# Kernel optimization log

Measured on AMD Instinct MI355X. Metric: run time of the kernel, lower is better.

Reference implementation:

```python
import jax, jax.numpy as jnp
import numpy as np

EPS = 1e-12  # matches torch.nn.functional.normalize eps


def setup_inputs() -> dict:
    key = jax.random.key(0)
    inputs = jax.random.normal(key, (128, 64, 64, 32), dtype=jnp.float32)
    return {"inputs": inputs}


def reference(inputs) -> jnp.ndarray:
    B, N = inputs.shape[0], inputs.shape[1]
    x = inputs.reshape(B, N, -1)                       # (B, N, D)
    norm = jnp.linalg.norm(x, axis=2, keepdims=True)   # (B, N, 1)
    att = x / jnp.maximum(norm, EPS)                   # L2-normalized rows
    # full N x N self-similarity per batch element
    sim = jnp.einsum('bnd,bmd->bnm', att, att)         # (B, N, N)
    diag_mean = (att * att).sum(axis=2).sum(axis=1).mean()
    loss = sim.sum(axis=(1, 2)).mean() - diag_mean
    return loss
```

## Files before the change

### kernel.cpp

```cpp
#include <hip/hip_runtime.h>
#include <math.h>

#define BB 128
#define NN 64
#define DD 2048
#define NBLK1 512
#define SEG 4

typedef float f4 __attribute__((ext_vector_type(4)));

__device__ __forceinline__ float wave_reduce_sum_down(float v) {
    #pragma unroll
    for (int off = 32; off > 0; off >>= 1)
        v += __shfl_down(v, off, 64);
    return v;
}

__global__ __launch_bounds__(256) void stream_kernel(
        const float* __restrict__ x,
        float* __restrict__ vseg,
        float* __restrict__ diag_seg,
        unsigned* __restrict__ counter) {
    const int u = blockIdx.x;
    const int b = u >> 2, s = u & 3;
    const int t = threadIdx.x;
    const int lane = t & 63, w = t >> 6;

    if (u == 0 && t == 0) *counter = 0;

    const float* xw = x + ((size_t)b * NN + s * 16 + w * 4) * DD;

    f4 a[4][8];
    #pragma unroll
    for (int r = 0; r < 4; ++r) {
        const f4* p = reinterpret_cast<const f4*>(xw + (size_t)r * DD);
        #pragma unroll
        for (int j = 0; j < 8; ++j)
            a[r][j] = __builtin_nontemporal_load(&p[lane + 64 * j]);
    }

    float ss[4];
    #pragma unroll
    for (int r = 0; r < 4; ++r) {
        float s4 = 0.f;
        #pragma unroll
        for (int j = 0; j < 8; ++j)
            s4 += a[r][j].x * a[r][j].x + a[r][j].y * a[r][j].y
                + a[r][j].z * a[r][j].z + a[r][j].w * a[r][j].w;
        ss[r] = s4;
    }

    #pragma unroll
    for (int off = 1; off < 64; off <<= 1) {
        float s0 = __shfl_xor(ss[0], off, 64);
        float s1 = __shfl_xor(ss[1], off, 64);
        float s2 = __shfl_xor(ss[2], off, 64);
        float s3 = __shfl_xor(ss[3], off, 64);
        ss[0] += s0; ss[1] += s1; ss[2] += s2; ss[3] += s3;
    }

    f4 acc[8];
    #pragma unroll
    for (int j = 0; j < 8; ++j) acc[j] = (f4)(0.f);
    float diag = 0.f;
    #pragma unroll
    for (int r = 0; r < 4; ++r) {
        const float inv = 1.0f / fmaxf(sqrtf(ss[r]), 1e-12f);
        diag += ss[r] * inv * inv;
        #pragma unroll
        for (int j = 0; j < 8; ++j) {
            acc[j].x = fmaf(a[r][j].x, inv, acc[j].x);
            acc[j].y = fmaf(a[r][j].y, inv, acc[j].y);
            acc[j].z = fmaf(a[r][j].z, inv, acc[j].z);
            acc[j].w = fmaf(a[r][j].w, inv, acc[j].w);
        }
    }

    __shared__ float lds[4][DD];
    __shared__ float dl[4];
    f4* lw = reinterpret_cast<f4*>(lds[w]);
    #pragma unroll
    for (int j = 0; j < 8; ++j) lw[lane + 64 * j] = acc[j];
    if (lane == 0) dl[w] = diag;
    __syncthreads();

    f4 o0 = (f4)(0.f);
    f4 o1 = (f4)(0.f);
    #pragma unroll
    for (int ww = 0; ww < 4; ++ww) {
        const f4* lr = reinterpret_cast<const f4*>(lds[ww]);
        f4 p0 = lr[t], p1 = lr[t + 256];
        o0 += p0;
        o1 += p1;
    }
    f4* dst = reinterpret_cast<f4*>(vseg + (size_t)u * DD);
    dst[t] = o0;
    dst[t + 256] = o1;
    if (t == 0) diag_seg[u] = dl[0] + dl[1] + dl[2] + dl[3];
}

__global__ __launch_bounds__(256) void combine_kernel(
        const float* __restrict__ vseg,
        const float* __restrict__ diag_seg,
        double* __restrict__ partials,
        unsigned* __restrict__ counter,
        float* __restrict__ out) {
    const int b = blockIdx.x;
    const int t = threadIdx.x;
    const int lane = t & 63, wid = t >> 6;

    __shared__ float red[4];
    __shared__ int flag;
    __shared__ double sd[BB];

    float4 c0 = make_float4(0.f, 0.f, 0.f, 0.f);
    float4 c1 = make_float4(0.f, 0.f, 0.f, 0.f);
    #pragma unroll
    for (int o = 0; o < SEG; ++o) {
        const float4* src = reinterpret_cast<const float4*>(
            vseg + (size_t)(b * SEG + o) * DD);
        float4 a0 = src[t], a1 = src[t + 256];
        c0.x += a0.x; c0.y += a0.y; c0.z += a0.z; c0.w += a0.w;
        c1.x += a1.x; c1.y += a1.y; c1.z += a1.z; c1.w += a1.w;
    }
    float p = c0.x * c0.x + c0.y * c0.y + c0.z * c0.z + c0.w * c0.w
            + c1.x * c1.x + c1.y * c1.y + c1.z * c1.z + c1.w * c1.w;
    p = wave_reduce_sum_down(p);
    if (lane == 0) red[wid] = p;
    __syncthreads();

    if (t == 0) {
        double sp = (double)red[0] + (double)red[1]
                  + (double)red[2] + (double)red[3];
        double dp = 0.0;
        #pragma unroll
        for (int o = 0; o < SEG; ++o) dp += (double)diag_seg[b * SEG + o];
        __hip_atomic_store(&partials[b], sp - dp,
                           __ATOMIC_RELAXED, __HIP_MEMORY_SCOPE_AGENT);
        asm volatile("s_waitcnt vmcnt(0)" ::: "memory");
        unsigned old = __hip_atomic_fetch_add(counter, 1u,
                        __ATOMIC_RELAXED, __HIP_MEMORY_SCOPE_AGENT);
        flag = (old == (unsigned)(BB - 1)) ? 1 : 0;
    }
    __syncthreads();
    if (!flag) return;

    if (t < BB)
        sd[t] = __hip_atomic_load(&partials[t],
                        __ATOMIC_RELAXED, __HIP_MEMORY_SCOPE_AGENT);
    __syncthreads();
    #pragma unroll
    for (int off = BB / 2; off > 0; off >>= 1) {
        if (t < off) sd[t] += sd[t + off];
        __syncthreads();
    }
    if (t == 0) out[0] = (float)(sd[0] / (double)BB);
}

extern "C" void kernel_launch(void* const* d_in, const int* in_sizes, int n_in,
                              void* d_out, int out_size, void* d_ws, size_t ws_size,
                              hipStream_t stream) {
    const float* x = (const float*)d_in[0];
    float* out = (float*)d_out;
    char* ws = (char*)d_ws;

    const size_t vbytes = (size_t)NBLK1 * DD * 4;
    float* vseg       = (float*)ws;
    float* diag_seg   = (float*)(ws + vbytes);
    double* partials  = (double*)(ws + vbytes + 2048);
    unsigned* counter = (unsigned*)(ws + vbytes + 2048 + 1024);

    stream_kernel<<<NBLK1, 256, 0, stream>>>(x, vseg, diag_seg, counter);
    combine_kernel<<<BB, 256, 0, stream>>>(vseg, diag_seg, partials,
                                           counter, out);
}
```

Measured before the change: 21.51 us.

## Fuse stream and combine kernels using per-batch last-block atomic counters

Merges the two launches into one kernel: each block writes its segment sum with coherent non-temporal stores, and the last of the four blocks for a batch (found with a per-batch atomic counter) reads the four segments back with cache-bypassing loads and does the combine. A global counter then picks the final reducer. Counters are reset with a hipMemsetAsync before the launch. This removes the second kernel launch and the gap between kernels, but adds a memset node plus extra atomics and fences.

```diff
diff --git a/kernel.cpp b/kernel.cpp
--- a/kernel.cpp
+++ b/kernel.cpp
@@ -4,7 +4,7 @@
 #define BB 128
 #define NN 64
 #define DD 2048
-#define NBLK1 512
+#define NBLK 512
 #define SEG 4
 
 typedef float f4 __attribute__((ext_vector_type(4)));
@@ -16,17 +16,23 @@
     return v;
 }
 
-__global__ __launch_bounds__(256) void stream_kernel(
+__device__ __forceinline__ void store_coherent(f4* p, f4 v) {
+    asm volatile("global_store_dwordx4 %0, %1, off sc0 sc1 nt"
+                 :: "v"(p), "v"(v) : "memory");
+}
+
+__global__ __launch_bounds__(256) void fused_kernel(
         const float* __restrict__ x,
         float* __restrict__ vseg,
-        float* __restrict__ diag_seg,
-        unsigned* __restrict__ counter) {
+        double* __restrict__ diag_seg,
+        double* __restrict__ partials,
+        unsigned* __restrict__ bcnt,
+        unsigned* __restrict__ gcnt,
+        float* __restrict__ out) {
     const int u = blockIdx.x;
     const int b = u >> 2, s = u & 3;
     const int t = threadIdx.x;
     const int lane = t & 63, w = t >> 6;
-
-    if (u == 0 && t == 0) *counter = 0;
 
     const float* xw = x + ((size_t)b * NN + s * 16 + w * 4) * DD;
 
@@ -78,73 +84,88 @@
 
     __shared__ float lds[4][DD];
     __shared__ float dl[4];
+    __shared__ float red[4];
+    __shared__ int flag;
     f4* lw = reinterpret_cast<f4*>(lds[w]);
     #pragma unroll
     for (int j = 0; j < 8; ++j) lw[lane + 64 * j] = acc[j];
     if (lane == 0) dl[w] = diag;
     __syncthreads();
 
-    f4 o0 = (f4)(0.f);
-    f4 o1 = (f4)(0.f);
+    f4 o0 = (f4)(0.f), o1 = (f4)(0.f);
     #pragma unroll
     for (int ww = 0; ww < 4; ++ww) {
         const f4* lr = reinterpret_cast<const f4*>(lds[ww]);
-        f4 p0 = lr[t], p1 = lr[t + 256];
-        o0 += p0;
-        o1 += p1;
+        o0 += lr[t];
+        o1 += lr[t + 256];
     }
     f4* dst = reinterpret_cast<f4*>(vseg + (size_t)u * DD);
-    dst[t] = o0;
-    dst[t + 256] = o1;
-    if (t == 0) diag_seg[u] = dl[0] + dl[1] + dl[2] + dl[3];
-}
-
-__global__ __launch_bounds__(256) void combine_kernel(
-        const float* __restrict__ vseg,
-        const float* __restrict__ diag_seg,
-        double* __restrict__ partials,
-        unsigned* __restrict__ counter,
-        float* __restrict__ out) {
-    const int b = blockIdx.x;
-    const int t = threadIdx.x;
-    const int lane = t & 63, wid = t >> 6;
-
-    __shared__ float red[4];
-    __shared__ int flag;
-    __shared__ double sd[BB];
-
-    float4 c0 = make_float4(0.f, 0.f, 0.f, 0.f);
-    float4 c1 = make_float4(0.f, 0.f, 0.f, 0.f);
-    #pragma unroll
-    for (int o = 0; o < SEG; ++o) {
-        const float4* src = reinterpret_cast<const float4*>(
-            vseg + (size_t)(b * SEG + o) * DD);
-        float4 a0 = src[t], a1 = src[t + 256];
-        c0.x += a0.x; c0.y += a0.y; c0.z += a0.z; c0.w += a0.w;
-        c1.x += a1.x; c1.y += a1.y; c1.z += a1.z; c1.w += a1.w;
-    }
-    float p = c0.x * c0.x + c0.y * c0.y + c0.z * c0.z + c0.w * c0.w
-            + c1.x * c1.x + c1.y * c1.y + c1.z * c1.z + c1.w * c1.w;
-    p = wave_reduce_sum_down(p);
-    if (lane == 0) red[wid] = p;
+    store_coherent(&dst[t], o0);
+    store_coherent(&dst[t + 256], o1);
+    if (t == 0)
+        __hip_atomic_store(&diag_seg[u],
+                           (double)dl[0] + dl[1] + dl[2] + dl[3],
+                           __ATOMIC_RELAXED, __HIP_MEMORY_SCOPE_AGENT);
+    asm volatile("s_waitcnt vmcnt(0)" ::: "memory");
     __syncthreads();
 
+    if (t == 0) {
+        unsigned old = __hip_atomic_fetch_add(&bcnt[b], 1u,
+                        __ATOMIC_RELAXED, __HIP_MEMORY_SCOPE_AGENT);
+        flag = (old == 3u) ? 1 : 0;
+    }
+    __syncthreads();
+    if (!flag) return;
+
+    {
+        const f4* s0p = reinterpret_cast<const f4*>(vseg + (size_t)(b * SEG + 0) * DD);
+        const f4* s1p = reinterpret_cast<const f4*>(vseg + (size_t)(b * SEG + 1) * DD);
+        const f4* s2p = reinterpret_cast<const f4*>(vseg + (size_t)(b * SEG + 2) * DD);
+        const f4* s3p = reinterpret_cast<const f4*>(vseg + (size_t)(b * SEG + 3) * DD);
+        f4 r0, r1, r2, r3, r4, r5, r6, r7;
+        asm volatile(
+            "global_load_dwordx4 %0, %8, off sc0 sc1\n\t"
+            "global_load_dwordx4 %1, %9, off sc0 sc1\n\t"
+            "global_load_dwordx4 %2, %10, off sc0 sc1\n\t"
+            "global_load_dwordx4 %3, %11, off sc0 sc1\n\t"
+            "global_load_dwordx4 %4, %12, off sc0 sc1\n\t"
+            "global_load_dwordx4 %5, %13, off sc0 sc1\n\t"
+            "global_load_dwordx4 %6, %14, off sc0 sc1\n\t"
+            "global_load_dwordx4 %7, %15, off sc0 sc1\n\t"
+            "s_waitcnt vmcnt(0)"
+            : "=&v"(r0), "=&v"(r1), "=&v"(r2), "=&v"(r3),
+              "=&v"(r4), "=&v"(r5), "=&v"(r6), "=&v"(r7)
+            : "v"(&s0p[t]), "v"(&s1p[t]), "v"(&s2p[t]), "v"(&s3p[t]),
+              "v"(&s0p[t + 256]), "v"(&s1p[t + 256]),
+              "v"(&s2p[t + 256]), "v"(&s3p[t + 256])
+            : "memory");
+        f4 c0 = r0 + r1 + r2 + r3;
+        f4 c1 = r4 + r5 + r6 + r7;
+        float p = c0.x * c0.x + c0.y * c0.y + c0.z * c0.z + c0.w * c0.w
+                + c1.x * c1.x + c1.y * c1.y + c1.z * c1.z + c1.w * c1.w;
+        p = wave_reduce_sum_down(p);
+        if (lane == 0) red[w] = p;
+    }
+    __syncthreads();
     if (t == 0) {
         double sp = (double)red[0] + (double)red[1]
                   + (double)red[2] + (double)red[3];
         double dp = 0.0;
         #pragma unroll
-        for (int o = 0; o < SEG; ++o) dp += (double)diag_seg[b * SEG + o];
+        for (int o = 0; o < SEG; ++o)
+            dp += __hip_atomic_load(&diag_seg[b * SEG + o],
+                        __ATOMIC_RELAXED, __HIP_MEMORY_SCOPE_AGENT);
         __hip_atomic_store(&partials[b], sp - dp,
                            __ATOMIC_RELAXED, __HIP_MEMORY_SCOPE_AGENT);
         asm volatile("s_waitcnt vmcnt(0)" ::: "memory");
-        unsigned old = __hip_atomic_fetch_add(counter, 1u,
+        unsigned old = __hip_atomic_fetch_add(gcnt, 1u,
                         __ATOMIC_RELAXED, __HIP_MEMORY_SCOPE_AGENT);
         flag = (old == (unsigned)(BB - 1)) ? 1 : 0;
     }
     __syncthreads();
     if (!flag) return;
 
+    __shared__ double sd[BB];
     if (t < BB)
         sd[t] = __hip_atomic_load(&partials[t],
                         __ATOMIC_RELAXED, __HIP_MEMORY_SCOPE_AGENT);
@@ -164,13 +185,14 @@
     float* out = (float*)d_out;
     char* ws = (char*)d_ws;
 
-    const size_t vbytes = (size_t)NBLK1 * DD * 4;
+    const size_t vbytes = (size_t)NBLK * DD * 4;
     float* vseg       = (float*)ws;
-    float* diag_seg   = (float*)(ws + vbytes);
-    double* partials  = (double*)(ws + vbytes + 2048);
-    unsigned* counter = (unsigned*)(ws + vbytes + 2048 + 1024);
+    double* diag_seg  = (double*)(ws + vbytes);
+    double* partials  = (double*)(ws + vbytes + 4096);
+    unsigned* bcnt    = (unsigned*)(ws + vbytes + 4096 + 1024);
+    unsigned* gcnt    = (unsigned*)(ws + vbytes + 4096 + 1024 + 512);
 
-    stream_kernel<<<NBLK1, 256, 0, stream>>>(x, vseg, diag_seg, counter);
-    combine_kernel<<<BB, 256, 0, stream>>>(vseg, diag_seg, partials,
-                                           counter, out);
+    hipMemsetAsync(bcnt, 0, 516, stream);
+    fused_kernel<<<NBLK, 256, 0, stream>>>(x, vseg, diag_seg, partials,
+                                           bcnt, gcnt, out);
 }
```

Measured after the change: 27.63 us. 1.28x slower.
